# Kernel optimization log

Measured on AMD Instinct MI355X. Metric: run time of the kernel, lower is better.

The kernel has to match this reference:

```python
import jax, jax.numpy as jnp
import numpy as np

N_NODES = 8192
NNZ = 131072

def spmm(idx, vals, M):
    # sparse (n,n) @ dense (n,m) -> (n,m) via edge-list gather + segment-sum
    rows, cols = idx[0], idx[1]
    return jax.ops.segment_sum(vals[:, None] * M[cols], rows, num_segments=N_NODES)

def gw_conv(A_list, X, Z, W):
    # X: (B, d, n) node features; Z: (n, dz); W: (d, out)
    B, d, n = X.shape
    X0 = X.reshape(-1, n)          # (B*d, n)
    Xt = X0.T                      # (n, B*d)
    total_t = Xt                   # sum over Chebyshev-order slices (batched path sums concat dim)
    for idx, vals in A_list:
        X1t = spmm(idx, vals, Xt)                 # order-1 diffusion
        X2t = 2.0 * spmm(idx, vals, X1t) - Xt     # Chebyshev order-2 recursion
        total_t = total_t + X1t + X2t
    # adaptive dense attention adjacency, softmax over dim 0 (columns)
    Az = jax.nn.softmax(jax.nn.relu(Z @ Z.T), axis=0)  # (n, n)
    total_t = total_t + Az @ Xt
    Xr = total_t.T.reshape(B, d, n).transpose(0, 2, 1)  # (B, n, d)
    return Xr @ W                                       # (B, n, out)

def setup_inputs() -> dict:
    key = jax.random.key(0)
    ks = jax.random.split(key, 8)
    d_in, h0, h1 = 64, 128, 128
    inp = {
        "A1_indices": jax.random.randint(ks[0], (2, NNZ), 0, N_NODES, dtype=jnp.int64) if jax.config.jax_enable_x64 else jax.random.randint(ks[0], (2, NNZ), 0, N_NODES, dtype=jnp.int32),
        "A1_values": jax.random.uniform(ks[1], (NNZ,), dtype=jnp.float32),
        "A2_indices": jax.random.randint(ks[2], (2, NNZ), 0, N_NODES, dtype=jnp.int32),
        "A2_values": jax.random.uniform(ks[3], (NNZ,), dtype=jnp.float32),
        "X": jax.random.normal(ks[4], (8, d_in, N_NODES), dtype=jnp.float32),
        "Z": jax.random.normal(ks[5], (N_NODES, 64), dtype=jnp.float32),
        "W1": jax.random.normal(ks[6], (d_in, h0), dtype=jnp.float32) / np.sqrt(h0),
        "W2": jax.random.normal(ks[7], (h0, h1), dtype=jnp.float32) / np.sqrt(h1),
    }
    return inp

def reference(A1_indices, A1_values, A2_indices, A2_values, X, Z, W1, W2):
    A = [(A1_indices, A1_values), (A2_indices, A2_values)]
    H = jax.nn.relu(gw_conv(A, X, Z, W1).transpose(0, 2, 1))  # (B, h0, n)
    H = jax.nn.relu(gw_conv(A, H, Z, W2).transpose(0, 2, 1))  # (B, h1, n)
    return H.mean(axis=2)                                     # aggregate over nodes -> (B, h1)
```

## Files before the change

### kernel.cpp

```cpp
#include <hip/hip_runtime.h>


#define NN 8192
#define NNZE 131072
#define CSHIFT 48.0f

typedef float4 f4;
typedef __attribute__((ext_vector_type(8))) short bf16x8;
typedef __attribute__((ext_vector_type(4))) float f32x4;

typedef __attribute__((address_space(3))) short lds_short;
typedef __attribute__((address_space(1))) const short glb_short;

struct P8s { short* p[8]; };

__device__ inline short f2b(float x){
  unsigned u = __float_as_uint(x);
  unsigned r = (u + 0x7fffu + ((u >> 16) & 1u)) >> 16;
  return (short)r;
}
__device__ inline float b2f(unsigned short b){
  return __uint_as_float(((unsigned)b) << 16);
}

__global__ __launch_bounds__(256) void k_count2(const int* __restrict__ i1, const int* __restrict__ i2,
                                                int* __restrict__ c1, int* __restrict__ c2){
  int e = blockIdx.x*256 + threadIdx.x;
  if (blockIdx.y == 0) atomicAdd(&c1[i1[e]], 1);
  else                 atomicAdd(&c2[i2[e]], 1);
}

__global__ __launch_bounds__(1024) void k_scan2(const int* __restrict__ cnt1, const int* __restrict__ cnt2,
                                                int* __restrict__ ptr1, int* __restrict__ ptr2,
                                                int* __restrict__ cur1, int* __restrict__ cur2){
  __shared__ int sums[1024];
  const int* cnt = blockIdx.x ? cnt2 : cnt1;
  int* ptr = blockIdx.x ? ptr2 : ptr1;
  int* cur = blockIdx.x ? cur2 : cur1;
  int t = threadIdx.x;
  int loc[8]; int s = 0;
  #pragma unroll
  for (int i=0;i<8;i++){ loc[i]=s; s += cnt[t*8+i]; }
  sums[t]=s; __syncthreads();
  for (int off=1; off<1024; off<<=1){
    int v = (t>=off) ? sums[t-off] : 0;
    __syncthreads();
    sums[t] += v;
    __syncthreads();
  }
  int excl = sums[t]-s;
  #pragma unroll
  for (int i=0;i<8;i++){ int v = excl + loc[i]; ptr[t*8+i] = v; cur[t*8+i] = v; }
  if (t==1023) ptr[NN] = sums[1023];
}

__global__ __launch_bounds__(256) void k_fill2(const int* __restrict__ i1, const float* __restrict__ v1,
                                               const int* __restrict__ i2, const float* __restrict__ v2,
                                               int* __restrict__ cur1, int* __restrict__ cur2,
                                               int* __restrict__ cidx1, float* __restrict__ cval1,
                                               int* __restrict__ cidx2, float* __restrict__ cval2){
  int e = blockIdx.x*256 + threadIdx.x;
  const int* idx; const float* vals; int* cur; int* cidx; float* cval;
  if (blockIdx.y == 0){ idx=i1; vals=v1; cur=cur1; cidx=cidx1; cval=cval1; }
  else                { idx=i2; vals=v2; cur=cur2; cidx=cidx2; cval=cval2; }
  int r = idx[e], c = idx[NNZE+e];
  int p = atomicAdd(&cur[r], 1);
  cidx[p] = c; cval[p] = vals[e];
}

template<int R>
__global__ __launch_bounds__(256) void k_transb(const float* __restrict__ src, short* __restrict__ dstb){
  __shared__ float tile[32][33];
  int tx = threadIdx.x & 31, ty = threadIdx.x >> 5;
  int j0 = blockIdx.x*32, f0 = blockIdx.y*32;
  #pragma unroll
  for (int u=0;u<32;u+=8) tile[ty+u][tx] = src[(size_t)(f0+ty+u)*NN + j0+tx];
  __syncthreads();
  #pragma unroll
  for (int u=0;u<32;u+=8) dstb[(size_t)(j0+ty+u)*R + f0+tx] = f2b(tile[tx][ty+u]);
}

__global__ __launch_bounds__(256) void k_zb(const float* __restrict__ Z, short* __restrict__ Zb){
  int i = blockIdx.x*256 + threadIdx.x;
  Zb[i] = f2b(Z[i]);
}

__global__ __launch_bounds__(256) void k_wt(const float* __restrict__ W1, const float* __restrict__ W2,
                                            short* __restrict__ W1t, short* __restrict__ W2t){
  int t = threadIdx.x;
  if (blockIdx.x == 0){
    for (int i=t; i<64*128; i+=256){ int k=i>>7, o=i&127; W1t[o*64+k] = f2b(W1[i]); }
  } else {
    for (int i=t; i<128*128; i+=256){ int k=i>>7, o=i&127; W2t[o*128+k] = f2b(W2[i]); }
  }
}

__global__ __launch_bounds__(512) void k_colsum_mfma(const short* __restrict__ Zb, float* __restrict__ sb){
  int t = threadIdx.x;
  int w = t >> 6, l = t & 63;
  int lo = l & 15, g = l >> 4;
  int j = blockIdx.x*128 + w*16 + lo;
  const bf16x8* Zb8 = (const bf16x8*)Zb;
  bf16x8 bj0 = Zb8[j*8 + g];
  bf16x8 bj1 = Zb8[j*8 + g + 4];
  int i0 = blockIdx.y * (NN/8);
  float sum = 0.f;
  for (int i = i0; i < i0 + NN/8; i += 16){
    bf16x8 a0 = Zb8[(size_t)(i+lo)*8 + g];
    bf16x8 a1 = Zb8[(size_t)(i+lo)*8 + g + 4];
    f32x4 s = (f32x4){0.f,0.f,0.f,0.f};
    s = __builtin_amdgcn_mfma_f32_16x16x32_bf16(a0, bj0, s, 0,0,0);
    s = __builtin_amdgcn_mfma_f32_16x16x32_bf16(a1, bj1, s, 0,0,0);
    #pragma unroll
    for (int r=0;r<4;r++) sum += __expf(s[r] - CSHIFT);
  }
  sum += __shfl_xor(sum, 16);
  sum += __shfl_xor(sum, 32);
  if (g == 0) atomicAdd(sb + j, sum);
}

__global__ __launch_bounds__(256) void k_scaleb(const float* __restrict__ X, const float* __restrict__ sb,
                                                short* __restrict__ Yt){
  int i = blockIdx.x*256 + threadIdx.x;
  int node4 = i & (NN/4 - 1);
  f4 x = ((const f4*)X)[i];
  f4 sv = ((const f4*)sb)[node4];
  short4 o;
  o.x = f2b(x.x*(1.0f/sv.x)); o.y = f2b(x.y*(1.0f/sv.y));
  o.z = f2b(x.z*(1.0f/sv.z)); o.w = f2b(x.w*(1.0f/sv.w));
  ((short4*)Yt)[i] = o;
}

template<int F, int MODE>
__global__ __launch_bounds__(512, 4) void k_fused(
    const short* __restrict__ Zb, const short* __restrict__ YS, P8s pp, int ksize, int kzbase, int nattn,
    const int* __restrict__ ptr1, const int* __restrict__ cidx1, const float* __restrict__ cval1,
    const int* __restrict__ ptr2, const int* __restrict__ cidx2, const float* __restrict__ cval2,
    const short* __restrict__ g1, const short* __restrict__ g2, const short* __restrict__ gy,
    short* __restrict__ so1, short* __restrict__ so2, float* __restrict__ T)
{
  __shared__ __align__(16) short zk[2][32*64];
  __shared__ __align__(16) short yt[2][256*32];
  __shared__ __align__(16) short p_lds[128*40];
  int t = threadIdx.x;

  if ((int)blockIdx.x < nattn){
    constexpr int NBY = F/256;
    int id = blockIdx.x;
    int bx = id & 63, rest = id >> 6;
    int m0 = bx * 128;
    int n0 = (rest % NBY) * 256;
    int kz = kzbase + rest / NBY;
    int kbeg = kz * ksize, kend = kbeg + ksize;
    int w = t >> 6, l = t & 63;
    int lo = l & 15, g = l >> 4;
    int wm = w >> 2, wn = w & 3;

    const bf16x8* Zb8 = (const bf16x8*)Zb;
    int zirow = m0 + w*16 + lo;
    bf16x8 ziA0 = Zb8[(size_t)zirow*8 + g];
    bf16x8 ziA1 = Zb8[(size_t)zirow*8 + g + 4];

    f32x4 acc[4][4];
    #pragma unroll
    for (int i=0;i<4;i++)
      #pragma unroll
      for (int j=0;j<4;j++) acc[i][j] = (f32x4){0.f,0.f,0.f,0.f};

    auto STAGE = [&](int b, int kk){
      if (t < 256){
        int r = t >> 3, c = t & 7;
        const short* src = Zb + (((size_t)(kk + r)) << 6) + ((c ^ (r & 7)) << 3);
        __builtin_amdgcn_global_load_lds((glb_short*)src, (lds_short*)&zk[b][t*8], 16, 0, 0);
      }
      #pragma unroll
      for (int p=0;p<2;p++){
        int cc = p*512 + t;
        int r = cc >> 2, c = cc & 3;
        const short* src = YS + (size_t)(n0 + r)*NN + kk + ((c ^ ((r >> 1) & 3)) << 3);
        __builtin_amdgcn_global_load_lds((glb_short*)src, (lds_short*)&yt[b][cc*8], 16, 0, 0);
      }
    };

    STAGE(0, kbeg);
    __syncthreads();

    int cur = 0;
    for (int k0 = kbeg; k0 < kend; k0 += 32){
      int xa = g ^ (lo & 7), xb = (g + 4) ^ (lo & 7);
      bf16x8 b00 = *(const bf16x8*)&zk[cur][(lo*8 + xa)*8];
      bf16x8 b01 = *(const bf16x8*)&zk[cur][(lo*8 + xb)*8];
      bf16x8 b10 = *(const bf16x8*)&zk[cur][((16+lo)*8 + xa)*8];
      bf16x8 b11 = *(const bf16x8*)&zk[cur][((16+lo)*8 + xb)*8];
      f32x4 s0 = (f32x4){0.f,0.f,0.f,0.f};
      f32x4 s1 = (f32x4){0.f,0.f,0.f,0.f};
      s0 = __builtin_amdgcn_mfma_f32_16x16x32_bf16(ziA0, b00, s0, 0,0,0);
      s0 = __builtin_amdgcn_mfma_f32_16x16x32_bf16(ziA1, b01, s0, 0,0,0);
      s1 = __builtin_amdgcn_mfma_f32_16x16x32_bf16(ziA0, b10, s1, 0,0,0);
      s1 = __builtin_amdgcn_mfma_f32_16x16x32_bf16(ziA1, b11, s1, 0,0,0);
      short e0[4], e1[4];
      #pragma unroll
      for (int r=0;r<4;r++){
        e0[r] = f2b(__expf(s0[r] - CSHIFT));
        e1[r] = f2b(__expf(s1[r] - CSHIFT));
      }
      __syncthreads();
      if (k0 + 32 < kend) STAGE(cur ^ 1, k0 + 32);
      int prow = w*16 + g*4;
      #pragma unroll
      for (int r=0;r<4;r++){
        p_lds[(prow+r)*40 + lo]      = e0[r];
        p_lds[(prow+r)*40 + 16 + lo] = e1[r];
      }
      __syncthreads();
      bf16x8 aP[4];
      #pragma unroll
      for (int mf=0; mf<4; mf++)
        aP[mf] = *(const bf16x8*)&p_lds[(wm*64 + mf*16 + lo)*40 + g*8];
      __builtin_amdgcn_s_setprio(1);
      #pragma unroll
      for (int nf=0; nf<4; nf++){
        int nl = wn*64 + nf*16 + lo;
        bf16x8 bY = *(const bf16x8*)&yt[cur][(nl*4 + (g ^ ((nl >> 1) & 3)))*8];
        #pragma unroll
        for (int mf=0; mf<4; mf++)
          acc[mf][nf] = __builtin_amdgcn_mfma_f32_16x16x32_bf16(aP[mf], bY, acc[mf][nf], 0,0,0);
      }
      __builtin_amdgcn_s_setprio(0);
      cur ^= 1;
    }
    short* outp = pp.p[kz];
    #pragma unroll
    for (int mf=0; mf<4; mf++){
      int row = m0 + wm*64 + mf*16 + g*4;
      #pragma unroll
      for (int nf=0; nf<4; nf++){
        int col = n0 + wn*64 + nf*16 + lo;
        #pragma unroll
        for (int r=0;r<4;r++)
          outp[(size_t)(row+r)*F + col] = f2b(acc[mf][nf][r]);
      }
    }
  } else {
    constexpr int LPR = F/8;
    constexpr int RPB = 512/LPR;
    int gid = blockIdx.x - nattn;
    int ts = t % LPR, rl = t / LPR;
    if (MODE == 0){
      constexpr int M = NN/RPB;
      int mat = gid / M;
      int blk = gid - mat*M;
      const int*   ptr  = mat ? ptr2  : ptr1;
      const int*   cidx = mat ? cidx2 : cidx1;
      const float* cval = mat ? cval2 : cval1;
      short* outb = mat ? so2 : so1;
      int r = blk*RPB + rl;
      const bf16x8* Y8 = (const bf16x8*)g1;
      int p0 = ptr[r], p1 = ptr[r+1];
      float a[8];
      #pragma unroll
      for (int j=0;j<8;j++) a[j]=0.f;
      int p = p0;
      for (; p+3 < p1; p += 4){
        int   c0=cidx[p], c1=cidx[p+1], c2=cidx[p+2], c3=cidx[p+3];
        float v0=cval[p], v1=cval[p+1], v2=cval[p+2], v3=cval[p+3];
        bf16x8 x0 = Y8[(size_t)c0*LPR + ts];
        bf16x8 x1 = Y8[(size_t)c1*LPR + ts];
        bf16x8 x2 = Y8[(size_t)c2*LPR + ts];
        bf16x8 x3 = Y8[(size_t)c3*LPR + ts];
        #pragma unroll
        for (int j=0;j<8;j++) a[j] += v0*b2f((unsigned short)x0[j]);
        #pragma unroll
        for (int j=0;j<8;j++) a[j] += v1*b2f((unsigned short)x1[j]);
        #pragma unroll
        for (int j=0;j<8;j++) a[j] += v2*b2f((unsigned short)x2[j]);
        #pragma unroll
        for (int j=0;j<8;j++) a[j] += v3*b2f((unsigned short)x3[j]);
      }
      for (; p < p1; ++p){
        int c0 = cidx[p]; float v0 = cval[p];
        bf16x8 x0 = Y8[(size_t)c0*LPR + ts];
        #pragma unroll
        for (int j=0;j<8;j++) a[j] += v0*b2f((unsigned short)x0[j]);
      }
      bf16x8 o;
      #pragma unroll
      for (int j=0;j<8;j++) o[j] = f2b(a[j]);
      ((bf16x8*)outb)[(size_t)r*LPR + ts] = o;
    } else {
      int r = gid*RPB + rl;
      const bf16x8* Xa = (const bf16x8*)g1;
      const bf16x8* Xb = (const bf16x8*)g2;
      float a[8];
      #pragma unroll
      for (int j=0;j<8;j++) a[j]=0.f;
      {
        int p0 = ptr1[r], p1 = ptr1[r+1];
        int p = p0;
        for (; p+3 < p1; p += 4){
          int   c0=cidx1[p], c1=cidx1[p+1], c2=cidx1[p+2], c3=cidx1[p+3];
          float v0=cval1[p], v1=cval1[p+1], v2=cval1[p+2], v3=cval1[p+3];
          bf16x8 x0 = Xa[(size_t)c0*LPR + ts];
          bf16x8 x1 = Xa[(size_t)c1*LPR + ts];
          bf16x8 x2 = Xa[(size_t)c2*LPR + ts];
          bf16x8 x3 = Xa[(size_t)c3*LPR + ts];
          #pragma unroll
          for (int j=0;j<8;j++) a[j] += v0*b2f((unsigned short)x0[j]);
          #pragma unroll
          for (int j=0;j<8;j++) a[j] += v1*b2f((unsigned short)x1[j]);
          #pragma unroll
          for (int j=0;j<8;j++) a[j] += v2*b2f((unsigned short)x2[j]);
          #pragma unroll
          for (int j=0;j<8;j++) a[j] += v3*b2f((unsigned short)x3[j]);
        }
        for (; p < p1; ++p){
          int c0 = cidx1[p]; float v0 = cval1[p];
          bf16x8 x0 = Xa[(size_t)c0*LPR + ts];
          #pragma unroll
          for (int j=0;j<8;j++) a[j] += v0*b2f((unsigned short)x0[j]);
        }
      }
      {
        int p0 = ptr2[r], p1 = ptr2[r+1];
        int p = p0;
        for (; p+3 < p1; p += 4){
          int   c0=cidx2[p], c1=cidx2[p+1], c2=cidx2[p+2], c3=cidx2[p+3];
          float v0=cval2[p], v1=cval2[p+1], v2=cval2[p+2], v3=cval2[p+3];
          bf16x8 x0 = Xb[(size_t)c0*LPR + ts];
          bf16x8 x1 = Xb[(size_t)c1*LPR + ts];
          bf16x8 x2 = Xb[(size_t)c2*LPR + ts];
          bf16x8 x3 = Xb[(size_t)c3*LPR + ts];
          #pragma unroll
          for (int j=0;j<8;j++) a[j] += v0*b2f((unsigned short)x0[j]);
          #pragma unroll
          for (int j=0;j<8;j++) a[j] += v1*b2f((unsigned short)x1[j]);
          #pragma unroll
          for (int j=0;j<8;j++) a[j] += v2*b2f((unsigned short)x2[j]);
          #pragma unroll
          for (int j=0;j<8;j++) a[j] += v3*b2f((unsigned short)x3[j]);
        }
        for (; p < p1; ++p){
          int c0 = cidx2[p]; float v0 = cval2[p];
          bf16x8 x0 = Xb[(size_t)c0*LPR + ts];
          #pragma unroll
          for (int j=0;j<8;j++) a[j] += v0*b2f((unsigned short)x0[j]);
        }
      }
      bf16x8 sa = Xa[(size_t)r*LPR + ts];
      bf16x8 sbv = Xb[(size_t)r*LPR + ts];
      bf16x8 yv = ((const bf16x8*)gy)[(size_t)r*LPR + ts];
      float o[8];
      #pragma unroll
      for (int j=0;j<8;j++)
        o[j] = 2.f*a[j] + b2f((unsigned short)sa[j]) + b2f((unsigned short)sbv[j]) - b2f((unsigned short)yv[j]);
      size_t o4 = ((size_t)r*F + ts*8) >> 2;
      ((f4*)T)[o4]   = (f4){o[0],o[1],o[2],o[3]};
      ((f4*)T)[o4+1] = (f4){o[4],o[5],o[6],o[7]};
    }
  }
}

__global__ __launch_bounds__(512) void k_headm_mfma(
    const float* __restrict__ T, P8s parts, const short* __restrict__ W1t,
    const float* __restrict__ sbv, short* __restrict__ Hb, short* __restrict__ Yt)
{
  __shared__ __align__(16) short hl[128*136];
  __shared__ float rsl[128];
  int t = threadIdx.x;
  int j0 = blockIdx.x*128, b = blockIdx.y;
  for (int u = t; u < 1024; u += 512){
    int row = u >> 3, c = u & 7;
    size_t base = (size_t)(j0+row)*512 + b*64 + c*8;
    f4 x0 = *(const f4*)(T + base);
    f4 x1 = *(const f4*)(T + base + 4);
    float v[8] = {x0.x,x0.y,x0.z,x0.w,x1.x,x1.y,x1.z,x1.w};
    #pragma unroll
    for (int j=0;j<4;j++){
      bf16x8 p = *(const bf16x8*)(parts.p[j] + base);
      #pragma unroll
      for (int q=0;q<8;q++) v[q] += b2f((unsigned short)p[q]);
    }
    bf16x8 o;
    #pragma unroll
    for (int q=0;q<8;q++) o[q] = f2b(v[q]);
    *(bf16x8*)&hl[(row*8 + (c ^ (row & 7)))*8] = o;
  }
  if (t < 128) rsl[t] = 1.0f / sbv[j0 + t];
  __syncthreads();
  int w = t >> 6, l = t & 63, lo = l & 15, g = l >> 4;
  int arow = w*16 + lo;
  f32x4 acc[8];
  #pragma unroll
  for (int nf=0;nf<8;nf++) acc[nf] = (f32x4){0.f,0.f,0.f,0.f};
  #pragma unroll
  for (int ks=0; ks<2; ks++){
    bf16x8 aA = *(const bf16x8*)&hl[(arow*8 + ((ks*4+g) ^ (arow & 7)))*8];
    #pragma unroll
    for (int nf=0; nf<8; nf++){
      bf16x8 bW = *(const bf16x8*)(W1t + (size_t)(nf*16+lo)*64 + ks*32 + g*8);
      acc[nf] = __builtin_amdgcn_mfma_f32_16x16x32_bf16(aA, bW, acc[nf], 0,0,0);
    }
  }
  __syncthreads();
  int m = w*16 + g*4;
  #pragma unroll
  for (int nf=0; nf<8; nf++){
    int o = nf*16 + lo;
    #pragma unroll
    for (int r=0;r<4;r++){
      short hv = f2b(fmaxf(acc[nf][r], 0.f));
      hl[o*136 + m + r] = hv;
      Hb[(size_t)(j0+m+r)*1024 + b*128 + o] = hv;
    }
  }
  __syncthreads();
  for (int u = t; u < 2048; u += 512){
    int o = u >> 4, m8 = (u & 15)*8;
    bf16x8 hv = *(const bf16x8*)&hl[o*136 + m8];
    bf16x8 ov;
    #pragma unroll
    for (int q=0;q<8;q++) ov[q] = f2b(b2f((unsigned short)hv[q]) * rsl[m8+q]);
    *(bf16x8*)(Yt + (size_t)(b*128+o)*NN + j0 + m8) = ov;
  }
}

__global__ __launch_bounds__(512) void k_heads_mfma(
    const float* __restrict__ T, P8s parts, const short* __restrict__ W2t,
    const float* __restrict__ W2unused, float* __restrict__ out)
{
  __shared__ __align__(16) short al[128*16*8];
  __shared__ float red[8*128];
  int t = threadIdx.x;
  int j0 = blockIdx.x*128, b = blockIdx.y;
  for (int u = t; u < 2048; u += 512){
    int row = u >> 4, c = u & 15;
    size_t base = (size_t)(j0+row)*1024 + b*128 + c*8;
    f4 x0 = *(const f4*)(T + base);
    f4 x1 = *(const f4*)(T + base + 4);
    float v[8] = {x0.x,x0.y,x0.z,x0.w,x1.x,x1.y,x1.z,x1.w};
    #pragma unroll
    for (int j=0;j<2;j++){
      bf16x8 p = *(const bf16x8*)(parts.p[j] + base);
      #pragma unroll
      for (int q=0;q<8;q++) v[q] += b2f((unsigned short)p[q]);
    }
    bf16x8 o;
    #pragma unroll
    for (int q=0;q<8;q++) o[q] = f2b(v[q]);
    *(bf16x8*)&al[(row*16 + (c ^ (row & 7)))*8] = o;
  }
  __syncthreads();
  int w = t >> 6, l = t & 63, lo = l & 15, g = l >> 4;
  int arow = w*16 + lo;
  f32x4 acc[8];
  #pragma unroll
  for (int nf=0;nf<8;nf++) acc[nf] = (f32x4){0.f,0.f,0.f,0.f};
  #pragma unroll
  for (int ks=0; ks<4; ks++){
    bf16x8 aA = *(const bf16x8*)&al[(arow*16 + ((ks*4+g) ^ (arow & 7)))*8];
    #pragma unroll
    for (int nf=0; nf<8; nf++){
      bf16x8 bW = *(const bf16x8*)(W2t + (size_t)(nf*16+lo)*128 + ks*32 + g*8);
      acc[nf] = __builtin_amdgcn_mfma_f32_16x16x32_bf16(aA, bW, acc[nf], 0,0,0);
    }
  }
  #pragma unroll
  for (int nf=0; nf<8; nf++){
    float s = fmaxf(acc[nf][0],0.f) + fmaxf(acc[nf][1],0.f)
            + fmaxf(acc[nf][2],0.f) + fmaxf(acc[nf][3],0.f);
    s += __shfl_xor(s, 16);
    s += __shfl_xor(s, 32);
    if (g == 0) red[w*128 + nf*16 + lo] = s;
  }
  __syncthreads();
  if (t < 128){
    float tot = 0.f;
    #pragma unroll
    for (int ww=0; ww<8; ww++) tot += red[ww*128 + t];
    atomicAdd(&out[b*128 + t], tot * (1.0f/8192.0f));
  }
}

extern "C" void kernel_launch(void* const* d_in, const int* in_sizes, int n_in,
                              void* d_out, int out_size, void* d_ws, size_t ws_size,
                              hipStream_t stream){
  const int*   A1i = (const int*)d_in[0];
  const float* A1v = (const float*)d_in[1];
  const int*   A2i = (const int*)d_in[2];
  const float* A2v = (const float*)d_in[3];
  const float* X   = (const float*)d_in[4];
  const float* Z   = (const float*)d_in[5];
  const float* W1  = (const float*)d_in[6];
  const float* W2  = (const float*)d_in[7];
  float* out = (float*)d_out;

  char* w = (char*)d_ws;
  size_t off = 0;
  auto alloc = [&](size_t b)->char* {
    char* p = w + off;
    off += (b + 1023) & ~(size_t)1023;
    return p;
  };
  const size_t MB = 1024*1024;
  float* sb    = (float*)alloc(NN*4);
  int*   ptr1  = (int*)  alloc((NN+1)*4);
  int*   ptr2  = (int*)  alloc((NN+1)*4);
  int*   cnt   = (int*)  alloc(2*NN*4);
  int*   cur1  = (int*)  alloc(NN*4);
  int*   cur2  = (int*)  alloc(NN*4);
  int*   cidx1 = (int*)  alloc(NNZE*4);
  float* cval1 = (float*)alloc(NNZE*4);
  int*   cidx2 = (int*)  alloc(NNZE*4);
  float* cval2 = (float*)alloc(NNZE*4);
  short* Zbf   = (short*)alloc((size_t)NN*64*2);
  short* W1t   = (short*)alloc(128*64*2);
  short* W2t   = (short*)alloc(128*128*2);
  short* XT1b  = (short*)alloc((size_t)NN*512*2);
  short* BUFA  = (short*)alloc((size_t)NN*1024*2);
  short* BUFB  = (short*)alloc((size_t)NN*1024*2);
  short* HTb   = (short*)alloc((size_t)NN*1024*2);
  short* YS    = (short*)alloc((size_t)NN*1024*2);
  float* T1    = (float*)alloc((size_t)NN*512*4);
  float* T2    = (float*)alloc((size_t)NN*1024*4);
  char*  PART  = alloc((size_t)32*MB);
  (void)ws_size;
  int* cnt1 = cnt;
  int* cnt2 = cnt + NN;

  hipMemsetAsync(cnt, 0, 2*NN*4, stream);
  k_count2<<<dim3(NNZE/256, 2), 256, 0, stream>>>(A1i, A2i, cnt1, cnt2);
  k_scan2<<<2, 1024, 0, stream>>>(cnt1, cnt2, ptr1, ptr2, cur1, cur2);
  k_fill2<<<dim3(NNZE/256, 2), 256, 0, stream>>>(A1i, A1v, A2i, A2v, cur1, cur2,
                                                 cidx1, cval1, cidx2, cval2);

  k_zb<<<NN*64/256, 256, 0, stream>>>(Z, Zbf);
  k_wt<<<2, 256, 0, stream>>>(W1, W2, W1t, W2t);
  hipMemsetAsync(sb, 0, NN*4, stream);
  hipMemsetAsync(out, 0, 1024*4, stream);
  k_colsum_mfma<<<dim3(NN/128, 8), 512, 0, stream>>>(Zbf, sb);
  k_transb<512><<<dim3(NN/32, 512/32), 256, 0, stream>>>(X, XT1b);
  k_scaleb<<<512*NN/4/256, 256, 0, stream>>>(X, sb, YS);

  P8s pp1{};
  for (int i=0;i<4;i++) pp1.p[i] = (short*)(PART + (size_t)i*8*MB);
  k_fused<512,0><<<256 + 2048, 512, 0, stream>>>(Zbf, YS, pp1, NN/4, 0, 256,
      ptr1, cidx1, cval1, ptr2, cidx2, cval2,
      XT1b, nullptr, nullptr, BUFA, BUFB, nullptr);
  k_fused<512,1><<<256 + 1024, 512, 0, stream>>>(Zbf, YS, pp1, NN/4, 2, 256,
      ptr1, cidx1, cval1, ptr2, cidx2, cval2,
      BUFA, BUFB, XT1b, nullptr, nullptr, T1);
  k_headm_mfma<<<dim3(NN/128, 8), 512, 0, stream>>>(T1, pp1, W1t, sb, HTb, YS);

  P8s pp2{};
  pp2.p[0] = (short*)PART;
  pp2.p[1] = (short*)(PART + (size_t)16*MB);
  k_fused<1024,0><<<256 + 4096, 512, 0, stream>>>(Zbf, YS, pp2, NN/2, 0, 256,
      ptr1, cidx1, cval1, ptr2, cidx2, cval2,
      HTb, nullptr, nullptr, BUFA, BUFB, nullptr);
  k_fused<1024,1><<<256 + 2048, 512, 0, stream>>>(Zbf, YS, pp2, NN/2, 1, 256,
      ptr1, cidx1, cval1, ptr2, cidx2, cval2,
      BUFA, BUFB, HTb, nullptr, nullptr, T2);
  k_heads_mfma<<<dim3(NN/128, 8), 512, 0, stream>>>(T2, pp2, W2t, W2, out);
}
```

Baseline: 596.7 us.

## Restructure attention pipeline barriers, remap block order, unroll SpMM gathers by eight

Fuses the attention branch's flash-style loop barriers, issuing the next stage's async LDS loads right after a vmcnt wait and barrier at the top of each iteration. This replaces two __syncthreads per step with an explicit waitcnt+barrier pair, and drops the register staging of the exp values. It also permutes the block index to change which tiles run concurrently, for better L2 locality. The CSR SpMM gather loops are unrolled from 4 to 8 nonzeros so more independent loads are in flight, at the cost of extra registers.

```diff
diff --git a/kernel.cpp b/kernel.cpp
--- a/kernel.cpp
+++ b/kernel.cpp
@@ -146,7 +146,8 @@
 
   if ((int)blockIdx.x < nattn){
     constexpr int NBY = F/256;
-    int id = blockIdx.x;
+    int id0 = blockIdx.x;
+    int id = (id0 & 7)*32 + (id0 >> 3);
     int bx = id & 63, rest = id >> 6;
     int m0 = bx * 128;
     int n0 = (rest % NBY) * 256;
@@ -183,10 +184,13 @@
     };
 
     STAGE(0, kbeg);
-    __syncthreads();
 
     int cur = 0;
     for (int k0 = kbeg; k0 < kend; k0 += 32){
+      asm volatile("s_waitcnt vmcnt(0)" ::: "memory");
+      __builtin_amdgcn_s_barrier();
+      __builtin_amdgcn_sched_barrier(0);
+      if (k0 + 32 < kend) STAGE(cur ^ 1, k0 + 32);
       int xa = g ^ (lo & 7), xb = (g + 4) ^ (lo & 7);
       bf16x8 b00 = *(const bf16x8*)&zk[cur][(lo*8 + xa)*8];
       bf16x8 b01 = *(const bf16x8*)&zk[cur][(lo*8 + xb)*8];
@@ -198,21 +202,14 @@
       s0 = __builtin_amdgcn_mfma_f32_16x16x32_bf16(ziA1, b01, s0, 0,0,0);
       s1 = __builtin_amdgcn_mfma_f32_16x16x32_bf16(ziA0, b10, s1, 0,0,0);
       s1 = __builtin_amdgcn_mfma_f32_16x16x32_bf16(ziA1, b11, s1, 0,0,0);
-      short e0[4], e1[4];
+      int prow = w*16 + g*4;
       #pragma unroll
       for (int r=0;r<4;r++){
-        e0[r] = f2b(__expf(s0[r] - CSHIFT));
-        e1[r] = f2b(__expf(s1[r] - CSHIFT));
-      }
-      __syncthreads();
-      if (k0 + 32 < kend) STAGE(cur ^ 1, k0 + 32);
-      int prow = w*16 + g*4;
-      #pragma unroll
-      for (int r=0;r<4;r++){
-        p_lds[(prow+r)*40 + lo]      = e0[r];
-        p_lds[(prow+r)*40 + 16 + lo] = e1[r];
-      }
-      __syncthreads();
+        p_lds[(prow+r)*40 + lo]      = f2b(__expf(s0[r] - CSHIFT));
+        p_lds[(prow+r)*40 + 16 + lo] = f2b(__expf(s1[r] - CSHIFT));
+      }
+      asm volatile("s_waitcnt lgkmcnt(0)" ::: "memory");
+      __builtin_amdgcn_s_barrier();
       bf16x8 aP[4];
       #pragma unroll
       for (int mf=0; mf<4; mf++)
@@ -261,21 +258,16 @@
       #pragma unroll
       for (int j=0;j<8;j++) a[j]=0.f;
       int p = p0;
-      for (; p+3 < p1; p += 4){
-        int   c0=cidx[p], c1=cidx[p+1], c2=cidx[p+2], c3=cidx[p+3];
-        float v0=cval[p], v1=cval[p+1], v2=cval[p+2], v3=cval[p+3];
-        bf16x8 x0 = Y8[(size_t)c0*LPR + ts];
-        bf16x8 x1 = Y8[(size_t)c1*LPR + ts];
-        bf16x8 x2 = Y8[(size_t)c2*LPR + ts];
-        bf16x8 x3 = Y8[(size_t)c3*LPR + ts];
+      for (; p+7 < p1; p += 8){
+        int   c[8]; float v[8]; bf16x8 x[8];
         #pragma unroll
-        for (int j=0;j<8;j++) a[j] += v0*b2f((unsigned short)x0[j]);
+        for (int q=0;q<8;q++){ c[q]=cidx[p+q]; v[q]=cval[p+q]; }
         #pragma unroll
-        for (int j=0;j<8;j++) a[j] += v1*b2f((unsigned short)x1[j]);
+        for (int q=0;q<8;q++) x[q] = Y8[(size_t)c[q]*LPR + ts];
         #pragma unroll
-        for (int j=0;j<8;j++) a[j] += v2*b2f((unsigned short)x2[j]);
-        #pragma unroll
-        for (int j=0;j<8;j++) a[j] += v3*b2f((unsigned short)x3[j]);
+        for (int q=0;q<8;q++)
+          #pragma unroll
+          for (int j=0;j<8;j++) a[j] += v[q]*b2f((unsigned short)x[q][j]);
       }
       for (; p < p1; ++p){
         int c0 = cidx[p]; float v0 = cval[p];
@@ -297,21 +289,16 @@
       {
         int p0 = ptr1[r], p1 = ptr1[r+1];
         int p = p0;
-        for (; p+3 < p1; p += 4){
-          int   c0=cidx1[p], c1=cidx1[p+1], c2=cidx1[p+2], c3=cidx1[p+3];
-          float v0=cval1[p], v1=cval1[p+1], v2=cval1[p+2], v3=cval1[p+3];
-          bf16x8 x0 = Xa[(size_t)c0*LPR + ts];
-          bf16x8 x1 = Xa[(size_t)c1*LPR + ts];
-          bf16x8 x2 = Xa[(size_t)c2*LPR + ts];
-          bf16x8 x3 = Xa[(size_t)c3*LPR + ts];
-          #pragma unroll
-          for (int j=0;j<8;j++) a[j] += v0*b2f((unsigned short)x0[j]);
-          #pragma unroll
-          for (int j=0;j<8;j++) a[j] += v1*b2f((unsigned short)x1[j]);
-          #pragma unroll
-          for (int j=0;j<8;j++) a[j] += v2*b2f((unsigned short)x2[j]);
-          #pragma unroll
-          for (int j=0;j<8;j++) a[j] += v3*b2f((unsigned short)x3[j]);
+        for (; p+7 < p1; p += 8){
+          int   c[8]; float v[8]; bf16x8 x[8];
+          #pragma unroll
+          for (int q=0;q<8;q++){ c[q]=cidx1[p+q]; v[q]=cval1[p+q]; }
+          #pragma unroll
+          for (int q=0;q<8;q++) x[q] = Xa[(size_t)c[q]*LPR + ts];
+          #pragma unroll
+          for (int q=0;q<8;q++)
+            #pragma unroll
+            for (int j=0;j<8;j++) a[j] += v[q]*b2f((unsigned short)x[q][j]);
         }
         for (; p < p1; ++p){
           int c0 = cidx1[p]; float v0 = cval1[p];
@@ -323,21 +310,16 @@
       {
         int p0 = ptr2[r], p1 = ptr2[r+1];
         int p = p0;
-        for (; p+3 < p1; p += 4){
-          int   c0=cidx2[p], c1=cidx2[p+1], c2=cidx2[p+2], c3=cidx2[p+3];
-          float v0=cval2[p], v1=cval2[p+1], v2=cval2[p+2], v3=cval2[p+3];
-          bf16x8 x0 = Xb[(size_t)c0*LPR + ts];
-          bf16x8 x1 = Xb[(size_t)c1*LPR + ts];
-          bf16x8 x2 = Xb[(size_t)c2*LPR + ts];
-          bf16x8 x3 = Xb[(size_t)c3*LPR + ts];
-          #pragma unroll
-          for (int j=0;j<8;j++) a[j] += v0*b2f((unsigned short)x0[j]);
-          #pragma unroll
-          for (int j=0;j<8;j++) a[j] += v1*b2f((unsigned short)x1[j]);
-          #pragma unroll
-          for (int j=0;j<8;j++) a[j] += v2*b2f((unsigned short)x2[j]);
-          #pragma unroll
-          for (int j=0;j<8;j++) a[j] += v3*b2f((unsigned short)x3[j]);
+        for (; p+7 < p1; p += 8){
+          int   c[8]; float v[8]; bf16x8 x[8];
+          #pragma unroll
+          for (int q=0;q<8;q++){ c[q]=cidx2[p+q]; v[q]=cval2[p+q]; }
+          #pragma unroll
+          for (int q=0;q<8;q++) x[q] = Xb[(size_t)c[q]*LPR + ts];
+          #pragma unroll
+          for (int q=0;q<8;q++)
+            #pragma unroll
+            for (int j=0;j<8;j++) a[j] += v[q]*b2f((unsigned short)x[q][j]);
         }
         for (; p < p1; ++p){
           int c0 = cidx2[p]; float v0 = cval2[p];
```

Result: faster. 545.4 us (-8.6%).
